# Kernel tuning notes

Hardware: AMD Instinct MI355X
Metric: run time of the kernel (lower is better)

Reference implementation:

```python
import jax, jax.numpy as jnp
import numpy as np

B, N, D = 4, 2048, 1024
THRESHOLD_FACTOR = 1.25


def setup_inputs() -> dict:
    key = jax.random.key(0)
    ks = jax.random.split(key, 8)
    s = 0.02  # init scale matching torch.randn * 0.02
    return {
        "hidden_states": jax.random.normal(ks[0], (B, N, D), jnp.float32),
        "Wq": jax.random.normal(ks[1], (D, D), jnp.float32) * s,
        "bq": jnp.zeros((D,), jnp.float32),
        "Wk": jax.random.normal(ks[2], (D, D), jnp.float32) * s,
        "bk": jnp.zeros((D,), jnp.float32),
        "Wv": jax.random.normal(ks[3], (D, D), jnp.float32) * s,
        "bv": jnp.zeros((D,), jnp.float32),
        "Wo": jax.random.normal(ks[4], (D, D), jnp.float32) * s,
        "bo": jnp.zeros((D,), jnp.float32),
        "Wtq": jax.random.normal(ks[5], (2, D), jnp.float32) * s,  # nn.Linear(D, 2)
        "btq": jnp.zeros((2,), jnp.float32),
        "Wfq": jax.random.normal(ks[6], (D, 2), jnp.float32) * s,  # HebbianLinear(2, D)
        "bfq": jnp.zeros((D,), jnp.float32),
    }


def _linear(x, W, b):
    return x @ W.T + b


def reference(hidden_states, Wq, bq, Wk, bk, Wv, bv, Wo, bo, Wtq, btq, Wfq, bfq):
    d = hidden_states.shape[-1]
    q = _linear(hidden_states, Wq, bq)
    k = _linear(hidden_states, Wk, bk)
    v = _linear(hidden_states, Wv, bv)
    scores = jnp.einsum('bid,bjd->bij', q, k) / jnp.sqrt(jnp.asarray(d, scores_dtype := q.dtype))

    # PhaseAwareBinaryAttention on 2-d quantum projection
    qp = _linear(hidden_states, Wtq, btq)            # [B, N, 2]
    diff = qp[:, :, None, :] - qp[:, None, :, :]      # [B, N, N, 2]
    dist_sq = jnp.sum(diff * diff, axis=-1)           # [B, N, N]
    phase_diff = jnp.arctan2(diff[..., 1], diff[..., 0])
    forward_bias = 0.5 * (1.0 + jnp.cos(phase_diff))
    mean_dist = jnp.mean(dist_sq, axis=(-1, -2), keepdims=True)
    std_dist = jnp.std(dist_sq, axis=(-1, -2), keepdims=True, ddof=1)  # torch unbiased std
    threshold = mean_dist + THRESHOLD_FACTOR * std_dist
    n = dist_sq.shape[-1]
    causal = jnp.tril(jnp.ones((n, n), bool))
    valid = (dist_sq <= threshold) & causal[None]
    binary_attn = valid.astype(scores.dtype) * forward_bias

    masked = jnp.where(binary_attn == 0, -jnp.inf, scores)
    weights = jax.nn.softmax(masked, axis=-1)
    context = jnp.einsum('bij,bjd->bid', weights, v)
    output = _linear(context, Wo, bo)

    # F.normalize(qp, p=2, dim=-1) with eps=1e-12
    r_embed = qp / jnp.maximum(jnp.linalg.norm(qp, axis=-1, keepdims=True), 1e-12)
    quantum_output = _linear(r_embed, Wfq, bfq)
    return hidden_states + output + 0.1 * quantum_output
```

## Files before the change

kernel.cpp:

```cpp
#include <hip/hip_runtime.h>
#include <math.h>

#define N_TOK 2048
#define DIM   1024
#define BATCH 4

typedef float v4f  __attribute__((ext_vector_type(4)));
typedef __bf16 v8bf __attribute__((ext_vector_type(8)));
typedef unsigned short v8us __attribute__((ext_vector_type(8)));

static __device__ __forceinline__ unsigned short f2bf(float f) {
  unsigned int u = __float_as_uint(f);
  u += 0x7fffu + ((u >> 16) & 1u);
  return (unsigned short)(u >> 16);
}
static __device__ __forceinline__ float bf2f(unsigned short h) {
  return __uint_as_float((unsigned int)h << 16);
}

__global__ __launch_bounds__(256) void castqp_kernel(
    const float* __restrict__ hs, const float* __restrict__ Wtq,
    const float* __restrict__ btq, unsigned short* __restrict__ hs_b,
    float2* __restrict__ qp, float2* __restrict__ remb) {
  int w = threadIdx.x >> 6, lane = threadIdx.x & 63;
  int row = blockIdx.x * 4 + w;
  const float* x = hs + (size_t)row * DIM;
  unsigned short* d = hs_b + (size_t)row * DIM;
  float a0 = 0.f, a1 = 0.f;
#pragma unroll
  for (int it = 0; it < 4; ++it) {
    int base = it * 256 + lane * 4;
    float4 v = *(const float4*)(x + base);
    float4 w0 = *(const float4*)(Wtq + base);
    float4 w1 = *(const float4*)(Wtq + DIM + base);
    ushort4 pk;
    pk.x = f2bf(v.x); pk.y = f2bf(v.y); pk.z = f2bf(v.z); pk.w = f2bf(v.w);
    *(ushort4*)(d + base) = pk;
    a0 += v.x * w0.x + v.y * w0.y + v.z * w0.z + v.w * w0.w;
    a1 += v.x * w1.x + v.y * w1.y + v.z * w1.z + v.w * w1.w;
  }
  for (int o = 32; o; o >>= 1) { a0 += __shfl_xor(a0, o); a1 += __shfl_xor(a1, o); }
  if (lane == 0) {
    a0 += btq[0]; a1 += btq[1];
    qp[row] = make_float2(a0, a1);
    float nrm = fmaxf(sqrtf(a0 * a0 + a1 * a1), 1e-12f);
    remb[row] = make_float2(a0 / nrm, a1 / nrm);
  }
}

__global__ __launch_bounds__(256) void cast_w4_kernel(
    const float* __restrict__ W0, const float* __restrict__ W1,
    const float* __restrict__ W2, const float* __restrict__ W3,
    unsigned short* __restrict__ D0, unsigned short* __restrict__ D1,
    unsigned short* __restrict__ D2, unsigned short* __restrict__ D3) {
  const float* s;
  unsigned short* d;
  switch (blockIdx.y) {
    case 0: s = W0; d = D0; break;
    case 1: s = W1; d = D1; break;
    case 2: s = W2; d = D2; break;
    default: s = W3; d = D3; break;
  }
  int i = (blockIdx.x * 256 + threadIdx.x) * 4;
  float4 v = *(const float4*)(s + i);
  d[i + 0] = f2bf(v.x); d[i + 1] = f2bf(v.y);
  d[i + 2] = f2bf(v.z); d[i + 3] = f2bf(v.w);
}

__global__ __launch_bounds__(256) void moments_kernel(
    const float2* __restrict__ qp, double* __restrict__ part) {
  int b = blockIdx.y;
  int i0 = blockIdx.x * 32;
  const float2* qb = qp + ((size_t)b << 11);
  double s1 = 0.0, s2 = 0.0;
  for (int idx = threadIdx.x; idx < 32 * N_TOK; idx += 256) {
    int i = i0 + (idx >> 11), j = idx & (N_TOK - 1);
    float2 pi = qb[i], pj = qb[j];
    float dx = pi.x - pj.x, dy = pi.y - pj.y;
    float dd = __fadd_rn(__fmul_rn(dx, dx), __fmul_rn(dy, dy));
    s1 += (double)dd;
    s2 += (double)dd * (double)dd;
  }
  int lane = threadIdx.x & 63, w = threadIdx.x >> 6;
  for (int o = 32; o; o >>= 1) { s1 += __shfl_xor(s1, o); s2 += __shfl_xor(s2, o); }
  __shared__ double red[8];
  if (lane == 0) { red[w] = s1; red[4 + w] = s2; }
  __syncthreads();
  if (threadIdx.x == 0) {
    int slot = b * 64 + blockIdx.x;
    part[slot * 2 + 0] = red[0] + red[1] + red[2] + red[3];
    part[slot * 2 + 1] = red[4] + red[5] + red[6] + red[7];
  }
}

__global__ __launch_bounds__(256) void thr_kernel(
    const double* __restrict__ part, float* __restrict__ thr) {
  int b = threadIdx.x >> 6, lane = threadIdx.x & 63;
  double s1 = part[(b * 64 + lane) * 2 + 0];
  double s2 = part[(b * 64 + lane) * 2 + 1];
  for (int o = 32; o; o >>= 1) { s1 += __shfl_xor(s1, o); s2 += __shfl_xor(s2, o); }
  if (lane == 0) {
    double n2 = (double)N_TOK * (double)N_TOK;
    double mean = s1 / n2;
    double var = (s2 - n2 * mean * mean) / (n2 - 1.0);
    if (var < 0.0) var = 0.0;
    thr[b] = (float)(mean + 1.25 * sqrt(var));
  }
}

__device__ __forceinline__ void gemm_ktile_loop(
    const unsigned short* __restrict__ Ag, const unsigned short* __restrict__ Bg,
    int ldA, int ldB, int kBeg, int kEnd,
    unsigned short* As, unsigned short* Bs, v4f acc[4][4]) {
  const int tid  = threadIdx.x;
  const int lane = tid & 63;
  const int wm   = ((tid >> 6) & 1) << 6, wn = (tid >> 7) << 6;
  const int quad = lane >> 4, l16 = lane & 15;
  const int srow = tid >> 3;
  const int scol = ((tid ^ srow) & 7) * 8;
  for (int k0 = kBeg; k0 < kEnd; k0 += 64) {
    __syncthreads();
#pragma unroll
    for (int it = 0; it < 4; ++it) {
      int row = srow + it * 32;
      const unsigned short* ga = Ag + (size_t)row * ldA + k0 + scol;
      const unsigned short* gb = Bg + (size_t)row * ldB + k0 + scol;
      unsigned short* la = As + (size_t)(it * 256 + (tid & ~63)) * 8;
      unsigned short* lb = Bs + (size_t)(it * 256 + (tid & ~63)) * 8;
      __builtin_amdgcn_global_load_lds((const __attribute__((address_space(1))) void*)ga,
                                       (__attribute__((address_space(3))) void*)la, 16, 0, 0);
      __builtin_amdgcn_global_load_lds((const __attribute__((address_space(1))) void*)gb,
                                       (__attribute__((address_space(3))) void*)lb, 16, 0, 0);
    }
    asm volatile("s_waitcnt vmcnt(0)" ::: "memory");
    __syncthreads();
#pragma unroll
    for (int kk = 0; kk < 64; kk += 32) {
      const int co = ((((kk >> 3) + quad) ^ (l16 & 7)) << 3);
      v8bf af[4], bfv[4];
#pragma unroll
      for (int i = 0; i < 4; ++i)
        af[i] = *(const v8bf*)(As + (wm + i * 16 + l16) * 64 + co);
#pragma unroll
      for (int i = 0; i < 4; ++i)
        bfv[i] = *(const v8bf*)(Bs + (wn + i * 16 + l16) * 64 + co);
#pragma unroll
      for (int mi = 0; mi < 4; ++mi)
#pragma unroll
        for (int ni = 0; ni < 4; ++ni)
          acc[mi][ni] = __builtin_amdgcn_mfma_f32_16x16x32_bf16(af[mi], bfv[ni], acc[mi][ni], 0, 0, 0);
    }
  }
}

__device__ __forceinline__ void ktile6464_loop(
    const unsigned short* __restrict__ Ag, const unsigned short* __restrict__ Bg,
    int ldA, int ldB, int kEnd,
    unsigned short* As, unsigned short* Bs, v4f acc[2][2]) {
  const int tid  = threadIdx.x;
  const int lane = tid & 63;
  const int wr   = ((tid >> 6) & 1) << 5, wc = (tid >> 7) << 5;
  const int quad = lane >> 4, l16 = lane & 15;
  const int srow = tid >> 3;
  const int scol = ((tid ^ srow) & 7) * 8;
  for (int k0 = 0; k0 < kEnd; k0 += 64) {
    __syncthreads();
#pragma unroll
    for (int it = 0; it < 2; ++it) {
      const unsigned short* ga = Ag + (size_t)(srow + it * 32) * ldA + k0 + scol;
      unsigned short* la = As + (size_t)(it * 256 + (tid & ~63)) * 8;
      __builtin_amdgcn_global_load_lds((const __attribute__((address_space(1))) void*)ga,
                                       (__attribute__((address_space(3))) void*)la, 16, 0, 0);
    }
#pragma unroll
    for (int it = 0; it < 2; ++it) {
      const unsigned short* gb = Bg + (size_t)(srow + it * 32) * ldB + k0 + scol;
      unsigned short* lb = Bs + (size_t)(it * 256 + (tid & ~63)) * 8;
      __builtin_amdgcn_global_load_lds((const __attribute__((address_space(1))) void*)gb,
                                       (__attribute__((address_space(3))) void*)lb, 16, 0, 0);
    }
    asm volatile("s_waitcnt vmcnt(0)" ::: "memory");
    __syncthreads();
#pragma unroll
    for (int kk = 0; kk < 64; kk += 32) {
      const int co = ((((kk >> 3) + quad) ^ (l16 & 7)) << 3);
      v8bf af[2], bfv[2];
#pragma unroll
      for (int i = 0; i < 2; ++i)
        af[i] = *(const v8bf*)(As + (wr + i * 16 + l16) * 64 + co);
#pragma unroll
      for (int i = 0; i < 2; ++i)
        bfv[i] = *(const v8bf*)(Bs + (wc + i * 16 + l16) * 64 + co);
#pragma unroll
      for (int mi = 0; mi < 2; ++mi)
#pragma unroll
        for (int ni = 0; ni < 2; ++ni)
          acc[mi][ni] = __builtin_amdgcn_mfma_f32_16x16x32_bf16(af[mi], bfv[ni], acc[mi][ni], 0, 0, 0);
    }
  }
}

#define PROLOG128                                                     \
  __shared__ __attribute__((aligned(16))) unsigned short smem[2][128 * 64];\
  unsigned short* As = smem[0];                                       \
  unsigned short* Bs = smem[1];                                       \
  v4f acc[4][4];                                                      \
  _Pragma("unroll") for (int i_ = 0; i_ < 4; ++i_)                    \
  _Pragma("unroll") for (int j_ = 0; j_ < 4; ++j_)                    \
      acc[i_][j_] = v4f{0.f, 0.f, 0.f, 0.f};                          \
  const int lane = threadIdx.x & 63, w = threadIdx.x >> 6;            \
  const int wm = (w & 1) << 6, wn = (w >> 1) << 6;                    \
  const int quad = lane >> 4, l16 = lane & 15;

#define PROLOG6464                                                    \
  __shared__ __attribute__((aligned(16))) unsigned short As[64 * 64]; \
  __shared__ __attribute__((aligned(16))) unsigned short Bs[64 * 64]; \
  v4f acc[2][2];                                                      \
  _Pragma("unroll") for (int i_ = 0; i_ < 2; ++i_)                    \
  _Pragma("unroll") for (int j_ = 0; j_ < 2; ++j_)                    \
      acc[i_][j_] = v4f{0.f, 0.f, 0.f, 0.f};                          \
  const int lane = threadIdx.x & 63, w = threadIdx.x >> 6;            \
  const int wr = (w & 1) << 5, wc = (w >> 1) << 5;                    \
  const int quad = lane >> 4, l16 = lane & 15;

__global__ __launch_bounds__(256) void gemm_qkv_fused_kernel(
    const unsigned short* __restrict__ X, const unsigned short* __restrict__ Wqkv,
    const float* __restrict__ bq, const float* __restrict__ bk,
    const float* __restrict__ bv, unsigned short* __restrict__ q_b,
    unsigned short* __restrict__ k_b, unsigned short* __restrict__ v_t) {
  PROLOG128
  int lid = blockIdx.y * 24 + blockIdx.x;
  int xcd = lid & 7, slot = lid >> 3;
  int by = (xcd << 3) | (slot & 7);
  int bx = slot >> 3;
  int m0 = by * 128, n0 = bx * 128;
  gemm_ktile_loop(X + (size_t)m0 * DIM, Wqkv + (size_t)n0 * DIM, DIM, DIM, 0, DIM, As, Bs, acc);
  int region = n0 >> 10;
  const float* bias = region == 0 ? bq : region == 1 ? bk : bv;
  int cbase = n0 & 1023;
  if (region < 2) {
    unsigned short* dst = region == 0 ? q_b : k_b;
#pragma unroll
    for (int mi = 0; mi < 4; ++mi) {
      int row0 = m0 + wm + mi * 16 + quad * 4;
#pragma unroll
      for (int ni = 0; ni < 4; ++ni) {
        int col = cbase + wn + ni * 16 + l16;
        float bcol = bias[col];
#pragma unroll
        for (int r = 0; r < 4; ++r)
          dst[(size_t)(row0 + r) * DIM + col] = f2bf(acc[mi][ni][r] + bcol);
      }
    }
  } else {
    unsigned short* T = &smem[0][0];
    __syncthreads();
#pragma unroll
    for (int mi = 0; mi < 4; ++mi) {
      int trow = wm + mi * 16 + quad * 4;
#pragma unroll
      for (int ni = 0; ni < 4; ++ni) {
        int fcol = wn + ni * 16 + l16;
        float bcol = bias[cbase + fcol];
        ushort4 pk;
        pk.x = f2bf(acc[mi][ni][0] + bcol);
        pk.y = f2bf(acc[mi][ni][1] + bcol);
        pk.z = f2bf(acc[mi][ni][2] + bcol);
        pk.w = f2bf(acc[mi][ni][3] + bcol);
        *(ushort4*)(T + fcol * 128 + trow) = pk;
      }
    }
    __syncthreads();
    int bb = m0 >> 11, tok0 = m0 & (N_TOK - 1);
    unsigned short* dstb = v_t + ((size_t)(bb << 10) + cbase) * N_TOK + tok0;
#pragma unroll
    for (int kk2 = 0; kk2 < 8; ++kk2) {
      int c = kk2 * 256 + threadIdx.x;
      int f = c >> 4, e0 = (c & 15) * 8;
      v8us v = *(const v8us*)(T + f * 128 + e0);
      *(v8us*)(dstb + (size_t)f * N_TOK + e0) = v;
    }
  }
}

__global__ __launch_bounds__(256) void gemm_scores_kernel(
    const unsigned short* __restrict__ q, const unsigned short* __restrict__ k,
    const float2* __restrict__ qp, const float* __restrict__ thr,
    unsigned short* __restrict__ S) {
  PROLOG6464
  int b = blockIdx.y;
  int bx = blockIdx.x;
  int t = (bx & 7) * 66 + (bx >> 3);
  int ti = (int)((sqrtf(8.f * (float)t + 1.f) - 1.f) * 0.5f);
  while ((ti + 1) * (ti + 2) / 2 <= t) ++ti;
  while (ti * (ti + 1) / 2 > t) --ti;
  int tj = t - ti * (ti + 1) / 2;
  int i0 = ti * 64, j0 = tj * 64;
  const unsigned short* qb = q + (size_t)b * N_TOK * DIM;
  const unsigned short* kb = k + (size_t)b * N_TOK * DIM;
  ktile6464_loop(qb + (size_t)i0 * DIM, kb + (size_t)j0 * DIM, DIM, DIM, DIM, As, Bs, acc);
  float th = thr[b];
  const float2* qpb = qp + ((size_t)b << 11);
  unsigned short* Sb = S + (size_t)b * N_TOK * N_TOK;
  float2 pjv[2];
#pragma unroll
  for (int ni = 0; ni < 2; ++ni) pjv[ni] = qpb[j0 + wc + ni * 16 + l16];
#pragma unroll
  for (int mi = 0; mi < 2; ++mi) {
#pragma unroll
    for (int r = 0; r < 4; ++r) {
      int i = i0 + wr + mi * 16 + quad * 4 + r;
      float2 pi2 = qpb[i];
#pragma unroll
      for (int ni = 0; ni < 2; ++ni) {
        int j = j0 + wc + ni * 16 + l16;
        if (j <= i) {
          float dx = pi2.x - pjv[ni].x, dy = pi2.y - pjv[ni].y;
          float dd = __fadd_rn(__fmul_rn(dx, dx), __fmul_rn(dy, dy));
          bool ok = (dd <= th);
          if (ok && dx < 0.f && fabsf(dy) <= 3e-4f * (-dx)) {
            float fb = 0.5f * (1.f + cosf(atan2f(dy, dx)));
            if (fb == 0.f) ok = false;
          }
          Sb[(size_t)i * N_TOK + j] = ok ? f2bf(acc[mi][ni][r] * 0.03125f) : 0xFF80;
        }
      }
    }
  }
}

__global__ __launch_bounds__(256) void softmax_kernel(
    const unsigned short* __restrict__ S, unsigned short* __restrict__ P) {
  int row = blockIdx.x;
  int b = row >> 11, i = row & (N_TOK - 1);
  const unsigned short* s = S + ((size_t)b * N_TOK + i) * N_TOK;
  unsigned short* p = P + ((size_t)b * N_TOK + i) * N_TOK;
  int tid = threadIdx.x, lane = tid & 63, w = tid >> 6;
  int lim = i + 1;
  int tail0 = lim & ~7, ntail = lim - tail0;
  __shared__ float redmax[4], redsum[4];
  float mx = -__builtin_inff();
  for (int j = tid * 8; j + 8 <= lim; j += 2048) {
    v8us v = *(const v8us*)(s + j);
#pragma unroll
    for (int e = 0; e < 8; ++e) mx = fmaxf(mx, bf2f(v[e]));
  }
  if (tid < ntail) mx = fmaxf(mx, bf2f(s[tail0 + tid]));
  for (int o = 32; o; o >>= 1) mx = fmaxf(mx, __shfl_xor(mx, o));
  if (lane == 0) redmax[w] = mx;
  __syncthreads();
  mx = fmaxf(fmaxf(redmax[0], redmax[1]), fmaxf(redmax[2], redmax[3]));
  float sum = 0.f;
  for (int j = tid * 8; j + 8 <= lim; j += 2048) {
    v8us v = *(const v8us*)(s + j);
#pragma unroll
    for (int e = 0; e < 8; ++e) sum += __expf(bf2f(v[e]) - mx);
  }
  if (tid < ntail) sum += __expf(bf2f(s[tail0 + tid]) - mx);
  for (int o = 32; o; o >>= 1) sum += __shfl_xor(sum, o);
  if (lane == 0) redsum[w] = sum;
  __syncthreads();
  sum = redsum[0] + redsum[1] + redsum[2] + redsum[3];
  float inv = 1.f / sum;
  for (int j = tid * 8; j + 8 <= lim; j += 2048) {
    v8us v = *(const v8us*)(s + j);
    v8us o;
#pragma unroll
    for (int e = 0; e < 8; ++e) o[e] = f2bf(__expf(bf2f(v[e]) - mx) * inv);
    *(v8us*)(p + j) = o;
  }
  if (tid < ntail) p[tail0 + tid] = f2bf(__expf(bf2f(s[tail0 + tid]) - mx) * inv);
  int zs = (lim + 7) & ~7;
  if (tid < zs - lim) p[lim + tid] = 0;
  v8us zv;
#pragma unroll
  for (int e = 0; e < 8; ++e) zv[e] = 0;
  for (int j = zs + tid * 8; j < N_TOK; j += 2048) *(v8us*)(p + j) = zv;
}

__global__ __launch_bounds__(256) void gemm_pv_kernel(
    const unsigned short* __restrict__ P, const unsigned short* __restrict__ vt,
    unsigned short* __restrict__ ctx) {
  PROLOG6464
  int b = blockIdx.z;
  int ti = blockIdx.y, d0 = blockIdx.x * 64;
  int i0 = ti * 64;
  const unsigned short* Pb = P + (size_t)b * N_TOK * N_TOK;
  const unsigned short* Vb = vt + ((size_t)b * DIM + d0) * N_TOK;
  int kEnd = (ti + 1) * 64;
  ktile6464_loop(Pb + (size_t)i0 * N_TOK, Vb, N_TOK, N_TOK, kEnd, As, Bs, acc);
#pragma unroll
  for (int mi = 0; mi < 2; ++mi) {
    int row0 = i0 + wr + mi * 16 + quad * 4;
#pragma unroll
    for (int ni = 0; ni < 2; ++ni) {
      int d = d0 + wc + ni * 16 + l16;
#pragma unroll
      for (int r = 0; r < 4; ++r)
        ctx[((size_t)b * N_TOK + row0 + r) * DIM + d] = f2bf(acc[mi][ni][r]);
    }
  }
}

__global__ __launch_bounds__(256) void gemm_out_kernel(
    const unsigned short* __restrict__ ctx, const unsigned short* __restrict__ Wob,
    const float* __restrict__ bo, const float* __restrict__ hs,
    const float2* __restrict__ remb, const float* __restrict__ Wfq,
    const float* __restrict__ bfq, float* __restrict__ out) {
  PROLOG6464
  int lid = blockIdx.y * 16 + blockIdx.x;
  int xcd = lid & 7, slot = lid >> 3;
  int by = (xcd << 4) | (slot & 15);
  int bx = slot >> 4;
  int m0 = by * 64, n0 = bx * 64;
  ktile6464_loop(ctx + (size_t)m0 * DIM, Wob + (size_t)n0 * DIM, DIM, DIM, DIM, As, Bs, acc);
#pragma unroll
  for (int mi = 0; mi < 2; ++mi) {
    int row0 = m0 + wr + mi * 16 + quad * 4;
#pragma unroll
    for (int ni = 0; ni < 2; ++ni) {
      int col = n0 + wc + ni * 16 + l16;
      float bias2 = bo[col] + 0.1f * bfq[col];
      float wf0 = 0.1f * Wfq[col * 2 + 0], wf1 = 0.1f * Wfq[col * 2 + 1];
#pragma unroll
      for (int r = 0; r < 4; ++r) {
        int row = row0 + r;
        float2 re = remb[row];
        out[(size_t)row * DIM + col] =
            acc[mi][ni][r] + bias2 + hs[(size_t)row * DIM + col] + re.x * wf0 + re.y * wf1;
      }
    }
  }
}

extern "C" void kernel_launch(void* const* d_in, const int* in_sizes, int n_in,
                              void* d_out, int out_size, void* d_ws, size_t ws_size,
                              hipStream_t stream) {
  const float* hs  = (const float*)d_in[0];
  const float* Wq  = (const float*)d_in[1];
  const float* bq  = (const float*)d_in[2];
  const float* Wk  = (const float*)d_in[3];
  const float* bk  = (const float*)d_in[4];
  const float* Wv  = (const float*)d_in[5];
  const float* bv  = (const float*)d_in[6];
  const float* Wo  = (const float*)d_in[7];
  const float* bo  = (const float*)d_in[8];
  const float* Wtq = (const float*)d_in[9];
  const float* btq = (const float*)d_in[10];
  const float* Wfq = (const float*)d_in[11];
  const float* bfq = (const float*)d_in[12];
  float* out = (float*)d_out;

  char* ws = (char*)d_ws;
  size_t off = 0;
  auto alloc = [&](size_t bytes) {
    char* p = ws + off;
    off += (bytes + 255) & ~(size_t)255;
    return p;
  };
  unsigned short* hs_b = (unsigned short*)alloc((size_t)8192 * 1024 * 2);
  unsigned short* q_b  = (unsigned short*)alloc((size_t)8192 * 1024 * 2);
  unsigned short* k_b  = (unsigned short*)alloc((size_t)8192 * 1024 * 2);
  unsigned short* v_t  = (unsigned short*)alloc((size_t)8192 * 1024 * 2);
  unsigned short* Wq_b = (unsigned short*)alloc((size_t)1024 * 1024 * 2);
  unsigned short* Wk_b = (unsigned short*)alloc((size_t)1024 * 1024 * 2);
  unsigned short* Wv_b = (unsigned short*)alloc((size_t)1024 * 1024 * 2);
  unsigned short* Wo_b = (unsigned short*)alloc((size_t)1024 * 1024 * 2);
  float2* qp   = (float2*)alloc((size_t)8192 * 8);
  float2* remb = (float2*)alloc((size_t)8192 * 8);
  double* part = (double*)alloc((size_t)BATCH * 64 * 2 * 8);
  float*  thr  = (float*)alloc(64);
  unsigned short* S = (unsigned short*)alloc((size_t)BATCH * N_TOK * N_TOK * 2);
  unsigned short* P   = q_b;
  unsigned short* ctx = hs_b;

  castqp_kernel<<<2048, 256, 0, stream>>>(hs, Wtq, btq, hs_b, qp, remb);
  cast_w4_kernel<<<dim3(1024, 4), 256, 0, stream>>>(Wq, Wk, Wv, Wo, Wq_b, Wk_b, Wv_b, Wo_b);
  moments_kernel<<<dim3(64, BATCH), 256, 0, stream>>>((const float2*)qp, part);
  thr_kernel<<<1, 256, 0, stream>>>(part, thr);

  gemm_qkv_fused_kernel<<<dim3(24, 64), 256, 0, stream>>>(
      hs_b, Wq_b, bq, bk, bv, q_b, k_b, v_t);

  gemm_scores_kernel<<<dim3(528, 4), 256, 0, stream>>>(
      q_b, k_b, (const float2*)qp, thr, S);

  softmax_kernel<<<8192, 256, 0, stream>>>(S, P);

  gemm_pv_kernel<<<dim3(16, 32, 4), 256, 0, stream>>>(P, v_t, ctx);

  gemm_out_kernel<<<dim3(16, 128), 256, 0, stream>>>(ctx, Wo_b, bo, hs, remb, Wfq, bfq, out);
}
```

Baseline: 341.9 us.

## Enlarge scores, PV and output GEMM tiles to 256-row blocks with 512 threads

Replaces the 64x64-tile GEMM loop used by the scores, PV and output-projection kernels with a templated 256xN tile loop (N = 256 or 128), run by 512-thread blocks where each wave computes 8xNFRAG MFMA fragments. The aim is more operand reuse per LDS load and fewer global reads of Q/K/P/V/ctx. In exchange the grids become much smaller (144 blocks for scores, 256 for PV and output), the XCD-aware block remapping is dropped, and triangular work per block is coarser. Register and LDS use per block rise sharply, which limits occupancy.

New measurement: 417.4 us. 1.22x slower.

```diff
diff --git a/kernel.cpp b/kernel.cpp
--- a/kernel.cpp
+++ b/kernel.cpp
@@ -153,53 +153,6 @@
   }
 }
 
-__device__ __forceinline__ void ktile6464_loop(
-    const unsigned short* __restrict__ Ag, const unsigned short* __restrict__ Bg,
-    int ldA, int ldB, int kEnd,
-    unsigned short* As, unsigned short* Bs, v4f acc[2][2]) {
-  const int tid  = threadIdx.x;
-  const int lane = tid & 63;
-  const int wr   = ((tid >> 6) & 1) << 5, wc = (tid >> 7) << 5;
-  const int quad = lane >> 4, l16 = lane & 15;
-  const int srow = tid >> 3;
-  const int scol = ((tid ^ srow) & 7) * 8;
-  for (int k0 = 0; k0 < kEnd; k0 += 64) {
-    __syncthreads();
-#pragma unroll
-    for (int it = 0; it < 2; ++it) {
-      const unsigned short* ga = Ag + (size_t)(srow + it * 32) * ldA + k0 + scol;
-      unsigned short* la = As + (size_t)(it * 256 + (tid & ~63)) * 8;
-      __builtin_amdgcn_global_load_lds((const __attribute__((address_space(1))) void*)ga,
-                                       (__attribute__((address_space(3))) void*)la, 16, 0, 0);
-    }
-#pragma unroll
-    for (int it = 0; it < 2; ++it) {
-      const unsigned short* gb = Bg + (size_t)(srow + it * 32) * ldB + k0 + scol;
-      unsigned short* lb = Bs + (size_t)(it * 256 + (tid & ~63)) * 8;
-      __builtin_amdgcn_global_load_lds((const __attribute__((address_space(1))) void*)gb,
-                                       (__attribute__((address_space(3))) void*)lb, 16, 0, 0);
-    }
-    asm volatile("s_waitcnt vmcnt(0)" ::: "memory");
-    __syncthreads();
-#pragma unroll
-    for (int kk = 0; kk < 64; kk += 32) {
-      const int co = ((((kk >> 3) + quad) ^ (l16 & 7)) << 3);
-      v8bf af[2], bfv[2];
-#pragma unroll
-      for (int i = 0; i < 2; ++i)
-        af[i] = *(const v8bf*)(As + (wr + i * 16 + l16) * 64 + co);
-#pragma unroll
-      for (int i = 0; i < 2; ++i)
-        bfv[i] = *(const v8bf*)(Bs + (wc + i * 16 + l16) * 64 + co);
-#pragma unroll
-      for (int mi = 0; mi < 2; ++mi)
-#pragma unroll
-        for (int ni = 0; ni < 2; ++ni)
-          acc[mi][ni] = __builtin_amdgcn_mfma_f32_16x16x32_bf16(af[mi], bfv[ni], acc[mi][ni], 0, 0, 0);
-    }
-  }
-}
-
 #define PROLOG128                                                     \
   __shared__ __attribute__((aligned(16))) unsigned short smem[2][128 * 64];\
   unsigned short* As = smem[0];                                       \
@@ -212,15 +165,74 @@
   const int wm = (w & 1) << 6, wn = (w >> 1) << 6;                    \
   const int quad = lane >> 4, l16 = lane & 15;
 
-#define PROLOG6464                                                    \
-  __shared__ __attribute__((aligned(16))) unsigned short As[64 * 64]; \
-  __shared__ __attribute__((aligned(16))) unsigned short Bs[64 * 64]; \
-  v4f acc[2][2];                                                      \
-  _Pragma("unroll") for (int i_ = 0; i_ < 2; ++i_)                    \
-  _Pragma("unroll") for (int j_ = 0; j_ < 2; ++j_)                    \
+template<int BROWS>
+__device__ __forceinline__ void stage_ab256(
+    const unsigned short* __restrict__ gA, const unsigned short* __restrict__ gB,
+    int ldA, int ldB, int k0, unsigned short* As, unsigned short* Bs) {
+  const int tid  = threadIdx.x;
+  const int srow = tid >> 3;
+  const int scol = ((tid ^ srow) & 7) * 8;
+  const int lbase = (tid & ~63) * 8;
+#pragma unroll
+  for (int it = 0; it < 4; ++it) {
+    const unsigned short* ga = gA + (size_t)(it * 64 + srow) * ldA + k0 + scol;
+    unsigned short* la = As + it * 4096 + lbase;
+    __builtin_amdgcn_global_load_lds((const __attribute__((address_space(1))) void*)ga,
+                                     (__attribute__((address_space(3))) void*)la, 16, 0, 0);
+  }
+#pragma unroll
+  for (int it = 0; it < BROWS / 64; ++it) {
+    const unsigned short* gb = gB + (size_t)(it * 64 + srow) * ldB + k0 + scol;
+    unsigned short* lb = Bs + it * 4096 + lbase;
+    __builtin_amdgcn_global_load_lds((const __attribute__((address_space(1))) void*)gb,
+                                     (__attribute__((address_space(3))) void*)lb, 16, 0, 0);
+  }
+}
+
+template<int NFRAG>
+__device__ __forceinline__ void compute_256(
+    const unsigned short* As, const unsigned short* Bs,
+    int wm_, int wn_, int quad, int l16, v4f (&acc)[8][NFRAG]) {
+#pragma unroll
+  for (int kk = 0; kk < 64; kk += 32) {
+    const int co = ((((kk >> 3) + quad) ^ (l16 & 7)) << 3);
+    v8bf af[8], bfv[NFRAG];
+#pragma unroll
+    for (int i = 0; i < 8; ++i)
+      af[i] = *(const v8bf*)(As + (wm_ + i * 16 + l16) * 64 + co);
+#pragma unroll
+    for (int i = 0; i < NFRAG; ++i)
+      bfv[i] = *(const v8bf*)(Bs + (wn_ + i * 16 + l16) * 64 + co);
+#pragma unroll
+    for (int mi = 0; mi < 8; ++mi)
+#pragma unroll
+      for (int ni = 0; ni < NFRAG; ++ni)
+        acc[mi][ni] = __builtin_amdgcn_mfma_f32_16x16x32_bf16(af[mi], bfv[ni], acc[mi][ni], 0, 0, 0);
+  }
+}
+
+template<int BROWS, int NFRAG>
+__device__ __forceinline__ void kloop_256sb(
+    const unsigned short* __restrict__ Ag, const unsigned short* __restrict__ Bg,
+    int ldA, int ldB, int kEnd,
+    unsigned short* As, unsigned short* Bs,
+    int wm_, int wn_, int quad, int l16, v4f (&acc)[8][NFRAG]) {
+  for (int k0 = 0; k0 < kEnd; k0 += 64) {
+    __syncthreads();
+    stage_ab256<BROWS>(Ag, Bg, ldA, ldB, k0, As, Bs);
+    asm volatile("s_waitcnt vmcnt(0)" ::: "memory");
+    __syncthreads();
+    compute_256<NFRAG>(As, Bs, wm_, wn_, quad, l16, acc);
+  }
+}
+
+#define PROLOG256(NF)                                                 \
+  v4f acc[8][NF];                                                     \
+  _Pragma("unroll") for (int i_ = 0; i_ < 8; ++i_)                    \
+  _Pragma("unroll") for (int j_ = 0; j_ < NF; ++j_)                   \
       acc[i_][j_] = v4f{0.f, 0.f, 0.f, 0.f};                          \
-  const int lane = threadIdx.x & 63, w = threadIdx.x >> 6;            \
-  const int wr = (w & 1) << 5, wc = (w >> 1) << 5;                    \
+  const int lane = threadIdx.x & 63, wid = threadIdx.x >> 6;          \
+  const int wm_ = (wid & 1) * 128, wn_ = (wid >> 1) * (NF * 16);      \
   const int quad = lane >> 4, l16 = lane & 15;
 
 __global__ __launch_bounds__(256) void gemm_qkv_fused_kernel(
@@ -283,37 +295,39 @@
   }
 }
 
-__global__ __launch_bounds__(256) void gemm_scores_kernel(
+__global__ __launch_bounds__(512, 2) void gemm_scores_kernel(
     const unsigned short* __restrict__ q, const unsigned short* __restrict__ k,
     const float2* __restrict__ qp, const float* __restrict__ thr,
     unsigned short* __restrict__ S) {
-  PROLOG6464
+  __shared__ __attribute__((aligned(16))) unsigned short sA[256 * 64];
+  __shared__ __attribute__((aligned(16))) unsigned short sB[256 * 64];
+  PROLOG256(4)
   int b = blockIdx.y;
-  int bx = blockIdx.x;
-  int t = (bx & 7) * 66 + (bx >> 3);
+  int t = blockIdx.x;
   int ti = (int)((sqrtf(8.f * (float)t + 1.f) - 1.f) * 0.5f);
   while ((ti + 1) * (ti + 2) / 2 <= t) ++ti;
   while (ti * (ti + 1) / 2 > t) --ti;
   int tj = t - ti * (ti + 1) / 2;
-  int i0 = ti * 64, j0 = tj * 64;
+  int i0 = ti * 256, j0 = tj * 256;
   const unsigned short* qb = q + (size_t)b * N_TOK * DIM;
   const unsigned short* kb = k + (size_t)b * N_TOK * DIM;
-  ktile6464_loop(qb + (size_t)i0 * DIM, kb + (size_t)j0 * DIM, DIM, DIM, DIM, As, Bs, acc);
+  kloop_256sb<256, 4>(qb + (size_t)i0 * DIM, kb + (size_t)j0 * DIM, DIM, DIM, DIM,
+                      sA, sB, wm_, wn_, quad, l16, acc);
   float th = thr[b];
   const float2* qpb = qp + ((size_t)b << 11);
   unsigned short* Sb = S + (size_t)b * N_TOK * N_TOK;
-  float2 pjv[2];
-#pragma unroll
-  for (int ni = 0; ni < 2; ++ni) pjv[ni] = qpb[j0 + wc + ni * 16 + l16];
-#pragma unroll
-  for (int mi = 0; mi < 2; ++mi) {
+  float2 pjv[4];
+#pragma unroll
+  for (int ni = 0; ni < 4; ++ni) pjv[ni] = qpb[j0 + wn_ + ni * 16 + l16];
+#pragma unroll
+  for (int mi = 0; mi < 8; ++mi) {
 #pragma unroll
     for (int r = 0; r < 4; ++r) {
-      int i = i0 + wr + mi * 16 + quad * 4 + r;
+      int i = i0 + wm_ + mi * 16 + quad * 4 + r;
       float2 pi2 = qpb[i];
 #pragma unroll
-      for (int ni = 0; ni < 2; ++ni) {
-        int j = j0 + wc + ni * 16 + l16;
+      for (int ni = 0; ni < 4; ++ni) {
+        int j = j0 + wn_ + ni * 16 + l16;
         if (j <= i) {
           float dx = pi2.x - pjv[ni].x, dy = pi2.y - pjv[ni].y;
           float dd = __fadd_rn(__fmul_rn(dx, dx), __fmul_rn(dy, dy));
@@ -378,23 +392,26 @@
   for (int j = zs + tid * 8; j < N_TOK; j += 2048) *(v8us*)(p + j) = zv;
 }
 
-__global__ __launch_bounds__(256) void gemm_pv_kernel(
+__global__ __launch_bounds__(512, 2) void gemm_pv_kernel(
     const unsigned short* __restrict__ P, const unsigned short* __restrict__ vt,
     unsigned short* __restrict__ ctx) {
-  PROLOG6464
+  __shared__ __attribute__((aligned(16))) unsigned short sA[256 * 64];
+  __shared__ __attribute__((aligned(16))) unsigned short sB[128 * 64];
+  PROLOG256(2)
   int b = blockIdx.z;
-  int ti = blockIdx.y, d0 = blockIdx.x * 64;
-  int i0 = ti * 64;
+  int ti = blockIdx.y, d0 = blockIdx.x * 128;
+  int i0 = ti * 256;
   const unsigned short* Pb = P + (size_t)b * N_TOK * N_TOK;
   const unsigned short* Vb = vt + ((size_t)b * DIM + d0) * N_TOK;
-  int kEnd = (ti + 1) * 64;
-  ktile6464_loop(Pb + (size_t)i0 * N_TOK, Vb, N_TOK, N_TOK, kEnd, As, Bs, acc);
-#pragma unroll
-  for (int mi = 0; mi < 2; ++mi) {
-    int row0 = i0 + wr + mi * 16 + quad * 4;
+  int kEnd = (ti + 1) * 256;
+  kloop_256sb<128, 2>(Pb + (size_t)i0 * N_TOK, Vb, N_TOK, N_TOK, kEnd,
+                      sA, sB, wm_, wn_, quad, l16, acc);
+#pragma unroll
+  for (int mi = 0; mi < 8; ++mi) {
+    int row0 = i0 + wm_ + mi * 16 + quad * 4;
 #pragma unroll
     for (int ni = 0; ni < 2; ++ni) {
-      int d = d0 + wc + ni * 16 + l16;
+      int d = d0 + wn_ + ni * 16 + l16;
 #pragma unroll
       for (int r = 0; r < 4; ++r)
         ctx[((size_t)b * N_TOK + row0 + r) * DIM + d] = f2bf(acc[mi][ni][r]);
@@ -402,24 +419,23 @@
   }
 }
 
-__global__ __launch_bounds__(256) void gemm_out_kernel(
+__global__ __launch_bounds__(512, 2) void gemm_out_kernel(
     const unsigned short* __restrict__ ctx, const unsigned short* __restrict__ Wob,
     const float* __restrict__ bo, const float* __restrict__ hs,
     const float2* __restrict__ remb, const float* __restrict__ Wfq,
     const float* __restrict__ bfq, float* __restrict__ out) {
-  PROLOG6464
-  int lid = blockIdx.y * 16 + blockIdx.x;
-  int xcd = lid & 7, slot = lid >> 3;
-  int by = (xcd << 4) | (slot & 15);
-  int bx = slot >> 4;
-  int m0 = by * 64, n0 = bx * 64;
-  ktile6464_loop(ctx + (size_t)m0 * DIM, Wob + (size_t)n0 * DIM, DIM, DIM, DIM, As, Bs, acc);
-#pragma unroll
-  for (int mi = 0; mi < 2; ++mi) {
-    int row0 = m0 + wr + mi * 16 + quad * 4;
+  __shared__ __attribute__((aligned(16))) unsigned short sA[256 * 64];
+  __shared__ __attribute__((aligned(16))) unsigned short sB[128 * 64];
+  PROLOG256(2)
+  int m0 = blockIdx.y * 256, n0 = blockIdx.x * 128;
+  kloop_256sb<128, 2>(ctx + (size_t)m0 * DIM, Wob + (size_t)n0 * DIM, DIM, DIM, DIM,
+                      sA, sB, wm_, wn_, quad, l16, acc);
+#pragma unroll
+  for (int mi = 0; mi < 8; ++mi) {
+    int row0 = m0 + wm_ + mi * 16 + quad * 4;
 #pragma unroll
     for (int ni = 0; ni < 2; ++ni) {
-      int col = n0 + wc + ni * 16 + l16;
+      int col = n0 + wn_ + ni * 16 + l16;
       float bias2 = bo[col] + 0.1f * bfq[col];
       float wf0 = 0.1f * Wfq[col * 2 + 0], wf1 = 0.1f * Wfq[col * 2 + 1];
 #pragma unroll
@@ -482,12 +498,12 @@
   gemm_qkv_fused_kernel<<<dim3(24, 64), 256, 0, stream>>>(
       hs_b, Wq_b, bq, bk, bv, q_b, k_b, v_t);
 
-  gemm_scores_kernel<<<dim3(528, 4), 256, 0, stream>>>(
+  gemm_scores_kernel<<<dim3(36, 4), 512, 0, stream>>>(
       q_b, k_b, (const float2*)qp, thr, S);
 
   softmax_kernel<<<8192, 256, 0, stream>>>(S, P);
 
-  gemm_pv_kernel<<<dim3(16, 32, 4), 256, 0, stream>>>(P, v_t, ctx);
-
-  gemm_out_kernel<<<dim3(16, 128), 256, 0, stream>>>(ctx, Wo_b, bo, hs, remb, Wfq, bfq, out);
-}
+  gemm_pv_kernel<<<dim3(8, 8, 4), 512, 0, stream>>>(P, v_t, ctx);
+
+  gemm_out_kernel<<<dim3(8, 32), 512, 0, stream>>>(ctx, Wo_b, bo, hs, remb, Wfq, bfq, out);
+}
```
